# Kernel optimization log

Measured on AMD Instinct MI355X. Metric: run time of the kernel, lower is better.

Reference implementation:

```python
import jax, jax.numpy as jnp
import numpy as np

N, E = 20000, 320000
CS, CV = 64, 32          # scalar / vector multiplicities of node (= node_pre) irreps
AS_, AV, H = 16, 8, 4    # attn irreps scalar/vector muls, num_heads
NB = 16                  # num_basis
SQRT3 = 1.7320508075688772
SQRT2 = 1.4142135623730951
EPS = 1e-5

# dtp weight layout: [ss(CS), sv(CS), vs(CV), vv0(CV), vv1(CV)] -> numel = 2*CS+3*CV = 224

def _cg_tp(s, v, y0, y1, w_ss, w_sv, w_vs, w_vv0, w_vv1):
    """Depthwise CG tensor product for l<=1.
    s:(E,CS) v:(E,CV,3) y0:(E,) y1:(E,3); weights (E,C) or (C,).
    out scalars (E, CS+CV): 0e x 0e -> 0e, 1o x 1o -> 0e (dot/sqrt3)
    out vectors (E, CS+2*CV, 3): 0e x 1o -> 1o, 1o x 0e -> 1o, 1o x 1o -> 1o (cross/sqrt2)
    """
    out_s = jnp.concatenate([
        w_ss * s * y0[:, None],
        w_vv0 * (jnp.einsum('eci,ei->ec', v, y1) / SQRT3)], axis=-1)
    out_v = jnp.concatenate([
        (w_sv * s)[:, :, None] * y1[:, None, :],
        (w_vs * jnp.ones_like(v[..., 0]))[..., None] * v * y0[:, None, None],
        (w_vv1 * jnp.ones_like(v[..., 0]))[..., None] * (jnp.cross(v, y1[:, None, :]) / SQRT2)], axis=1)
    return out_s, out_v


def _equiv_layernorm(s, v, gamma_s, beta_s, gamma_v):
    mu = jnp.mean(s, axis=-1, keepdims=True)
    var = jnp.var(s, axis=-1, keepdims=True)
    s_n = (s - mu) * jax.lax.rsqrt(var + EPS) * gamma_s + beta_s
    rms = jnp.sqrt(jnp.mean(jnp.sum(v * v, axis=-1), axis=-1, keepdims=True) + EPS)
    v_n = v / rms[..., None] * gamma_v[None, :, None]
    return s_n, v_n


def setup_inputs() -> dict:
    key = jax.random.key(0)
    ks = jax.random.split(key, 26)
    def rn(k, shape, fan):
        return jax.random.normal(k, shape, jnp.float32) / np.sqrt(fan)
    D1S, D1V = CS + CV, CS + 2 * CV          # 96, 128 (dtp output muls)
    WN = 2 * CS + 3 * CV                     # 224 dtp weight numel
    inp = {
        'node': jax.random.normal(ks[0], (N, CS + 3 * CV), jnp.float32),
        'edge_index': jax.random.randint(ks[1], (2, E), 0, N, jnp.int64 if jax.config.jax_enable_x64 else jnp.int32),
        'rbf': jax.random.uniform(ks[2], (E, NB), jnp.float32),
        'rsh': jax.random.normal(ks[3], (E, 4), jnp.float32),
        'gamma_s': jnp.ones((CS,), jnp.float32),
        'beta_s': jnp.zeros((CS,), jnp.float32),
        'gamma_v': jnp.ones((CV,), jnp.float32),
        'Ws_src': rn(ks[4], (CS, CS), CS), 'Wv_src': rn(ks[5], (CV, CV), CV),
        'Ws_dst': rn(ks[6], (CS, CS), CS), 'Wv_dst': rn(ks[7], (CV, CV), CV),
        'W_rbf': rn(ks[8], (NB, WN), NB),
        'W_alpha': rn(ks[9], (D1S, H * AS_), D1S),
        'alpha_dot': rn(ks[10], (1, H, AS_), AS_),
        'Ws_val': rn(ks[11], (D1S, CS), D1S), 'Wv_val': rn(ks[12], (D1V, CV), D1V),
        'Wg': rn(ks[13], (CS, CV), CS),
        'w2_ss': rn(ks[14], (CS,), 1), 'w2_sv': rn(ks[15], (CS,), 1),
        'w2_vs': rn(ks[16], (CV,), 1), 'w2_vv0': rn(ks[17], (CV,), 1), 'w2_vv1': rn(ks[18], (CV,), 1),
        'Ws_vlin': rn(ks[19], (D1S, H * AS_), D1S), 'Wv_vlin': rn(ks[20], (D1V, H * AV), D1V),
        'Wps': rn(ks[21], (H * AS_, CS), H * AS_), 'Wpv': rn(ks[22], (H * AV, CV), H * AV),
    }
    return inp


def reference(node, rbf, rsh, gamma_s, beta_s, gamma_v, Ws_src, Wv_src, Ws_dst, Wv_dst,
              W_rbf, W_alpha, alpha_dot, Ws_val, Wv_val, Wg,
              w2_ss, w2_sv, w2_vs, w2_vv0, w2_vv1, Ws_vlin, Wv_vlin, Wps, Wpv, edge_index):
    n = node.shape[0]
    e = rsh.shape[0]
    s = node[:, :CS]
    v = node[:, CS:].reshape(n, CV, 3)
    # equivariant layer norm
    s_n, v_n = _equiv_layernorm(s, v, gamma_s, beta_s, gamma_v)
    # merge_src / merge_dst (irrep-wise o3.Linear)
    src, dst = edge_index[0], edge_index[1]
    msg_s = (s_n @ Ws_src)[src] + (s_n @ Ws_dst)[dst]                       # (E,CS)
    msg_v = jnp.einsum('ncx,cd->ndx', v_n, Wv_src)[src] + \
            jnp.einsum('ncx,cd->ndx', v_n, Wv_dst)[dst]                     # (E,CV,3)
    y0, y1 = rsh[:, 0], rsh[:, 1:4]
    # dtp1: per-edge weighted CG coupling, weights from rbf
    w1 = rbf @ W_rbf                                                        # (E,224)
    m1_s, m1_v = _cg_tp(msg_s, msg_v, y0, y1,
                        w1[:, :CS], w1[:, CS:2*CS], w1[:, 2*CS:2*CS+CV],
                        w1[:, 2*CS+CV:2*CS+2*CV], w1[:, 2*CS+2*CV:])        # (E,96) (E,128,3)
    # attention logits
    a = (m1_s @ W_alpha).reshape(e, H, AS_)
    a = jnp.where(a > 0, a, 0.2 * a)                                        # LeakyReLU(0.2)
    a = jnp.sum(a * alpha_dot, axis=-1, keepdims=True)                      # (E,H,1)
    # softmax over incoming edges of each destination node
    amax = jax.ops.segment_max(a, dst, num_segments=n)
    amax = jnp.where(jnp.isfinite(amax), amax, 0.0)
    ex = jnp.exp(a - amax[dst])
    den = jax.ops.segment_sum(ex, dst, num_segments=n)
    alpha = ex / (den[dst] + 1e-16)                                         # (E,H,1)
    # value path
    val_s = m1_s @ Ws_val                                                   # (E,CS)
    val_v = jnp.einsum('ecx,cd->edx', m1_v, Wv_val)                         # (E,CV,3)
    # gate: sigmoid on scalars, vectors gated by sigmoid of learned scalar gates
    val_v = val_v * jax.nn.sigmoid(val_s @ Wg)[..., None]
    val_s = jax.nn.sigmoid(val_s)
    # dtp2: shared internal weights
    m2_s, m2_v = _cg_tp(val_s, val_v, y0, y1, w2_ss, w2_sv, w2_vs, w2_vv0, w2_vv1)
    # value_lin -> (attn_irreps * num_heads), head-major layout
    hs = (m2_s @ Ws_vlin).reshape(e, H, AS_)
    hv = jnp.einsum('ecx,cd->edx', m2_v, Wv_vlin).reshape(e, H, AV, 3)
    h = jnp.concatenate([hs, hv.reshape(e, H, AV * 3)], axis=-1)            # (E,H,40)
    # attend + scatter-add to destination nodes
    agg = jax.ops.segment_sum(alpha * h, dst, num_segments=n)               # (N,H,40)
    agg_s = agg[:, :, :AS_].reshape(n, H * AS_)                             # (N,64)
    agg_v = agg[:, :, AS_:].reshape(n, H * AV, 3)                           # (N,32,3)
    out = node + jnp.concatenate([
        agg_s @ Wps,
        jnp.einsum('ncx,cd->ndx', agg_v, Wpv).reshape(n, CV * 3)], axis=-1)
    return out
```

## Files before the change

kernel.cpp:

```cpp
#include <hip/hip_runtime.h>
#include <hip/hip_bf16.h>
#include <cstddef>

typedef __hip_bfloat16 bf16;
typedef __bf16 bfv8 __attribute__((ext_vector_type(8)));
typedef __bf16 bfv4 __attribute__((ext_vector_type(4)));
typedef float f4 __attribute__((ext_vector_type(4)));

#define EPSN 1e-5f
#define SQRT3_INV 0.57735026918962576f
#define SQRT2_INV 0.70710678118654752f

__device__ __forceinline__ float b2f(bf16 x) { return __bfloat162float(x); }

template<int BF> __device__ __forceinline__ float ldf(const void* p, size_t i) {
    if (BF) return __bfloat162float(((const bf16*)p)[i]);
    return ((const float*)p)[i];
}
__device__ __forceinline__ float ldr(const void* p, size_t i, int bfm) {
    return bfm ? __bfloat162float(((const bf16*)p)[i]) : ((const float*)p)[i];
}
template<int BF> __device__ __forceinline__ void stf(void* p, size_t i, float v) {
    if (BF) ((bf16*)p)[i] = __float2bfloat16(v);
    else    ((float*)p)[i] = v;
}

__device__ __forceinline__ float wave_sum64(float x) {
    #pragma unroll
    for (int m = 1; m < 64; m <<= 1) x += __shfl_xor(x, m, 64);
    return x;
}

__device__ __forceinline__ f4 mf(bfv8 a, bfv8 b, f4 c) {
    return __builtin_amdgcn_mfma_f32_16x16x32_bf16(a, b, c, 0, 0, 0);
}

__global__ __launch_bounds__(256) void k_sniff(const void* node, const void* eidx, int* flags)
{
    int t = threadIdx.x;
    __shared__ int cnt;
    __shared__ unsigned orr;
    if (t == 0) { cnt = 0; orr = 0u; }
    __syncthreads();
    unsigned w  = ((const unsigned*)node)[t];
    unsigned lo = w & 0xFFFFu;
    int e_lo = (int)((lo >> 7) & 0xFF);
    if (e_lo >= 96 && e_lo <= 140) atomicAdd(&cnt, 1);
    unsigned odd = ((const unsigned*)eidx)[2 * t + 1];
    atomicOr(&orr, odd);
    __syncthreads();
    if (t == 0) {
        flags[0] = (cnt >= 128) ? 1 : 0;
        flags[1] = (orr == 0u) ? 1 : 0;
    }
}

__global__ __launch_bounds__(256) void k_zero(float* p, int n)
{
    int i = blockIdx.x * 256 + threadIdx.x;
    if (i < n) p[i] = 0.f;
}

__global__ __launch_bounds__(256) void k_hist(const void* eidx, int* cnt,
                                              const int* flags, int E)
{
    int e = blockIdx.x * 256 + threadIdx.x;
    if (e >= E) return;
    int d = flags[1] ? (int)((const long long*)eidx)[(long long)E + e]
                     : ((const int*)eidx)[(size_t)E + e];
    atomicAdd(&cnt[d], 1);
}

__global__ __launch_bounds__(1024) void k_scan(int* cnt, int N)
{
    __shared__ int wsum[16];
    int t = threadIdx.x;
    int lane = t & 63, w = t >> 6;
    int chunk = (N + 1023) >> 10;
    int lo = t * chunk, hi = lo + chunk;
    if (hi > N) hi = N; if (lo > N) lo = N;
    int sum = 0;
    for (int i = lo; i < hi; ++i) sum += cnt[i];
    int x = sum;
    #pragma unroll
    for (int off = 1; off < 64; off <<= 1) {
        int y = __shfl_up(x, off, 64);
        if (lane >= off) x += y;
    }
    if (lane == 63) wsum[w] = x;
    __syncthreads();
    if (t < 64) {
        int v = (lane < 16) ? wsum[lane] : 0;
        #pragma unroll
        for (int off = 1; off < 16; off <<= 1) {
            int y = __shfl_up(v, off, 64);
            if (lane >= off) v += y;
        }
        if (lane < 16) wsum[lane] = v;
    }
    __syncthreads();
    int acc = x - sum + (w ? wsum[w - 1] : 0);
    for (int i = lo; i < hi; ++i) { int v = cnt[i]; cnt[i] = acc; acc += v; }
}

__global__ __launch_bounds__(256) void k_perm(const void* eidx, int* cnt, int* perm,
                                              const int* flags, int E)
{
    int e = blockIdx.x * 256 + threadIdx.x;
    if (e >= E) return;
    int d = flags[1] ? (int)((const long long*)eidx)[(long long)E + e]
                     : ((const int*)eidx)[(size_t)E + e];
    int pos = atomicAdd(&cnt[d], 1);
    perm[pos] = e;
}

template<int BF>
__device__ __forceinline__ void prep_impl(
    const void* Walpha, const void* Wsval, const void* Wsvlin,
    const void* Wvval, const void* Wvvlin, const void* Wg,
    const void* Wrbf, const void* adot,
    const void* w2ss, const void* w2sv, const void* w2vs,
    const void* w2vv0, const void* w2vv1,
    bf16* WalphaT, bf16* WsvalT, bf16* WsvlinT,
    bf16* WvvalT, bf16* WvvlinT, bf16* WgT,
    bf16* WrbfT, bf16* adotB, bf16* w2B)
{
    int t = threadIdx.x + blockIdx.x * 256;
    int T = gridDim.x * 256;
    for (int i = t; i < 96 * 64; i += T) {
        int c = i >> 6, n = i & 63;
        WalphaT[n * 96 + c] = __float2bfloat16(ldf<BF>(Walpha, i));
        WsvalT [n * 96 + c] = __float2bfloat16(ldf<BF>(Wsval,  i));
        WsvlinT[n * 96 + c] = __float2bfloat16(ldf<BF>(Wsvlin, i));
    }
    for (int i = t; i < 128 * 32; i += T) {
        int c = i >> 5, n = i & 31;
        WvvalT [n * 128 + c] = __float2bfloat16(ldf<BF>(Wvval,  i));
        WvvlinT[n * 128 + c] = __float2bfloat16(ldf<BF>(Wvvlin, i));
    }
    for (int i = t; i < 64 * 32; i += T) {
        int c = i >> 5, n = i & 31;
        WgT[n * 64 + c] = __float2bfloat16(ldf<BF>(Wg, i));
    }
    for (int i = t; i < 224 * 32; i += T) {
        int c = i >> 5, b = i & 31;
        WrbfT[i] = __float2bfloat16(b < 16 ? ldf<BF>(Wrbf, b * 224 + c) : 0.f);
    }
    if (t < 64) adotB[t] = __float2bfloat16(ldf<BF>(adot, t));
    if (t < 64) w2B[t]      = __float2bfloat16(ldf<BF>(w2ss, t));
    if (t < 64) w2B[64 + t] = __float2bfloat16(ldf<BF>(w2sv, t));
    if (t < 32) {
        w2B[128 + t] = __float2bfloat16(ldf<BF>(w2vs, t));
        w2B[160 + t] = __float2bfloat16(ldf<BF>(w2vv0, t));
        w2B[192 + t] = __float2bfloat16(ldf<BF>(w2vv1, t));
    }
}

__global__ __launch_bounds__(256) void k_prep(
    const void* Walpha, const void* Wsval, const void* Wsvlin,
    const void* Wvval, const void* Wvvlin, const void* Wg,
    const void* Wrbf, const void* adot,
    const void* w2ss, const void* w2sv, const void* w2vs,
    const void* w2vv0, const void* w2vv1,
    bf16* WalphaT, bf16* WsvalT, bf16* WsvlinT,
    bf16* WvvalT, bf16* WvvlinT, bf16* WgT,
    bf16* WrbfT, bf16* adotB, bf16* w2B, const int* flags)
{
    if (flags[0])
        prep_impl<1>(Walpha, Wsval, Wsvlin, Wvval, Wvvlin, Wg, Wrbf, adot,
                     w2ss, w2sv, w2vs, w2vv0, w2vv1,
                     WalphaT, WsvalT, WsvlinT, WvvalT, WvvlinT, WgT, WrbfT, adotB, w2B);
    else
        prep_impl<0>(Walpha, Wsval, Wsvlin, Wvval, Wvvlin, Wg, Wrbf, adot,
                     w2ss, w2sv, w2vs, w2vv0, w2vv1,
                     WalphaT, WsvalT, WsvlinT, WvvalT, WvvlinT, WgT, WrbfT, adotB, w2B);
}

template<int BF>
__device__ __forceinline__ void node_impl(
    const void* node, const void* gs, const void* bs, const void* gv,
    const void* Wss, const void* Wvs, const void* Wsd, const void* Wvd,
    bf16* ssrc, bf16* sdst, bf16* vsrc, bf16* vdst,
    float* shs, float* shv, int n, int lane)
{
    size_t nb = (size_t)n * 160;

    float s  = ldf<BF>(node, nb + lane);
    float mu = wave_sum64(s) * (1.f / 64.f);
    float d  = s - mu;
    float var = wave_sum64(d * d) * (1.f / 64.f);
    float sn  = d * rsqrtf(var + EPSN) * ldf<BF>(gs, lane) + ldf<BF>(bs, lane);
    shs[lane] = sn;

    float v0 = 0.f, v1 = 0.f, v2 = 0.f, qq = 0.f;
    if (lane < 32) {
        v0 = ldf<BF>(node, nb + 64 + lane * 3 + 0);
        v1 = ldf<BF>(node, nb + 64 + lane * 3 + 1);
        v2 = ldf<BF>(node, nb + 64 + lane * 3 + 2);
        qq = v0 * v0 + v1 * v1 + v2 * v2;
    }
    float msq = wave_sum64(qq) * (1.f / 32.f);
    float inv = rsqrtf(msq + EPSN);
    if (lane < 32) {
        float g = ldf<BF>(gv, lane);
        shv[0 * 32 + lane] = v0 * inv * g;
        shv[1 * 32 + lane] = v1 * inv * g;
        shv[2 * 32 + lane] = v2 * inv * g;
    }

    float a1 = 0.f, a2 = 0.f;
    for (int c = 0; c < 64; ++c) {
        float sc = shs[c];
        a1 += sc * ldf<BF>(Wss, c * 64 + lane);
        a2 += sc * ldf<BF>(Wsd, c * 64 + lane);
    }
    {
        int cs = lane;
        int pos = (cs & 15) * 4 + (cs >> 4);
        ssrc[(size_t)n * 64 + pos] = __float2bfloat16(a1);
        sdst[(size_t)n * 64 + pos] = __float2bfloat16(a2);
    }

    {
        int x = lane >> 5, dd = lane & 31;
        float p1 = 0.f, p2 = 0.f;
        for (int c = 0; c < 32; ++c) {
            float vc = shv[x * 32 + c];
            p1 += vc * ldf<BF>(Wvs, c * 32 + dd);
            p2 += vc * ldf<BF>(Wvd, c * 32 + dd);
        }
        int cv = x * 32 + dd;
        int pos = (cv & 15) * 8 + (cv >> 4);
        vsrc[(size_t)n * 128 + pos] = __float2bfloat16(p1);
        vdst[(size_t)n * 128 + pos] = __float2bfloat16(p2);
    }
    if (lane < 32) {
        int dd = lane;
        float p1 = 0.f, p2 = 0.f;
        for (int c = 0; c < 32; ++c) {
            float vc = shv[2 * 32 + c];
            p1 += vc * ldf<BF>(Wvs, c * 32 + dd);
            p2 += vc * ldf<BF>(Wvd, c * 32 + dd);
        }
        int cv = 64 + dd;
        int pos = (cv & 15) * 8 + (cv >> 4);
        vsrc[(size_t)n * 128 + pos] = __float2bfloat16(p1);
        vdst[(size_t)n * 128 + pos] = __float2bfloat16(p2);
    }
}

__global__ __launch_bounds__(256) void k_node(
    const void* node, const void* gs, const void* bs, const void* gv,
    const void* Wss, const void* Wvs, const void* Wsd, const void* Wvd,
    bf16* ssrc, bf16* sdst, bf16* vsrc, bf16* vdst,
    const int* flags, int N)
{
    __shared__ float shs[4][64];
    __shared__ float shv[4][96];
    int wv = threadIdx.x >> 6, lane = threadIdx.x & 63;
    int n = blockIdx.x * 4 + wv; if (n >= N) return;
    if (flags[0])
        node_impl<1>(node, gs, bs, gv, Wss, Wvs, Wsd, Wvd, ssrc, sdst, vsrc, vdst,
                     shs[wv], shv[wv], n, lane);
    else
        node_impl<0>(node, gs, bs, gv, Wss, Wvs, Wsd, Wvd, ssrc, sdst, vsrc, vdst,
                     shs[wv], shv[wv], n, lane);
}

static constexpr int SS  = 104;
static constexpr int A1S = 0;
static constexpr int SV  = 136;
static constexpr int P0  = 16 * SS;
static constexpr int P1  = P0 + 16 * SV;
static constexpr int VAL = 0;
static constexpr int SA  = 72;
static constexpr int HSZ = P1 + 16 * SV;

#define W_M1(X, PB) do { \
    constexpr int x_ = (X), x1_ = ((X)+1)%3, x2_ = ((X)+2)%3; \
    _Pragma("unroll") \
    for (int r = 0; r < 4; ++r) { \
        int e = q * 4 + r; \
        float4 yy = *(const float4*)&sY[wv][e][0]; \
        float y0 = yy.x; float yv[3] = {yy.y, yy.z, yy.w}; \
        _Pragma("unroll") \
        for (int nt = 0; nt < 4; ++nt) \
            H[(PB) + e * SV + nt * 16 + m] = (__bf16)(sv_[r][nt] * yv[x_]); \
        _Pragma("unroll") \
        for (int n2 = 0; n2 < 2; ++n2) { \
            int c = 64 + n2 * 16 + m; \
            H[(PB) + e * SV + c] = (__bf16)(qv_[r][n2][x_] * y0); \
            float cr = pv_[r][n2][x1_] * yv[x2_] - pv_[r][n2][x2_] * yv[x1_]; \
            H[(PB) + e * SV + 32 + c] = (__bf16)(cr * SQRT2_INV); \
        } \
    } \
} while (0)

#define W_M2(X, PB) do { \
    constexpr int x_ = (X), x1_ = ((X)+1)%3, x2_ = ((X)+2)%3; \
    _Pragma("unroll") \
    for (int r = 0; r < 4; ++r) { \
        int e = q * 4 + r; \
        float4 yy = *(const float4*)&sY[wv][e][0]; \
        float y0 = yy.x; float yv[3] = {yy.y, yy.z, yy.w}; \
        _Pragma("unroll") \
        for (int nt = 0; nt < 4; ++nt) \
            H[(PB) + e * SV + nt * 16 + m] = (__bf16)(c2sv[nt] * vals[nt][r] * yv[x_]); \
        _Pragma("unroll") \
        for (int n2 = 0; n2 < 2; ++n2) { \
            int c = 64 + n2 * 16 + m; \
            H[(PB) + e * SV + c] = (__bf16)(c2vs[n2] * vv[x_][n2][r] * y0); \
            float cr = vv[x1_][n2][r] * yv[x2_] - vv[x2_][n2][r] * yv[x1_]; \
            H[(PB) + e * SV + 32 + c] = (__bf16)(c2v1[n2] * cr * SQRT2_INV); \
        } \
    } \
} while (0)

#define MMA_V(PB, WB, O0, O1) do { \
    bfv8 fg_[4]; \
    _Pragma("unroll") \
    for (int kt = 0; kt < 4; ++kt) \
        fg_[kt] = *(const bfv8*)(H + (PB) + m * SV + kt * 32 + kq); \
    _Pragma("unroll") \
    for (int kt = 0; kt < 4; ++kt) { \
        O0 = mf(fg_[kt], *(const bfv8*)((WB) + (size_t)(0 * 16 + m) * 128 + kt * 32 + kq), O0); \
        O1 = mf(fg_[kt], *(const bfv8*)((WB) + (size_t)(1 * 16 + m) * 128 + kt * 32 + kq), O1); \
    } \
} while (0)

__global__ __launch_bounds__(256, 3) void k_edge(
    const void* __restrict__ eidx, const void* __restrict__ rbf, const void* __restrict__ rsh,
    const bf16* __restrict__ WalphaT, const bf16* __restrict__ WsvalT, const bf16* __restrict__ WsvlinT,
    const bf16* __restrict__ WvvalT, const bf16* __restrict__ WvvlinT, const bf16* __restrict__ WgT,
    const bf16* __restrict__ WrbfT, const bf16* __restrict__ adotB, const bf16* __restrict__ w2B,
    const bf16* __restrict__ ssrc, const bf16* __restrict__ sdst,
    const bf16* __restrict__ vsrc, const bf16* __restrict__ vdst,
    const int* __restrict__ perm,
    float* __restrict__ den, float* __restrict__ agg,
    const int* __restrict__ flags, int E)
{
    const int bfm = flags[0];
    const int i64 = flags[1];

    __shared__ __align__(16) __bf16 sH[4][HSZ];
    __shared__ __align__(16) float sY[4][16][4];
    __shared__ int sSD[4][48];

    int wv = threadIdx.x >> 6, l = threadIdx.x & 63;
    int q = l >> 4, m = l & 15;
    const int kq = q * 8;
    long long eb = ((long long)blockIdx.x * 4 + wv) * 16;
    if (eb >= E) return;
    __bf16* H = &sH[wv][0];

    if (l < 16) {
        long long p = eb + l; if (p > (long long)E - 1) p = E - 1;
        sSD[wv][32 + l] = perm[p];
    }
    if (l < 32) {
        int pe = sSD[wv][32 + (l & 15)];
        long long off = (l < 16) ? (long long)pe : ((long long)E + pe);
        sSD[wv][l] = i64 ? (int)((const long long*)eidx)[off] : ((const int*)eidx)[off];
    }
    {
        int pe = sSD[wv][32 + (l >> 2)];
        sY[wv][l >> 2][l & 3] = ldr(rsh, (size_t)pe * 4 + (l & 3), bfm);
    }

    f4 w1f[14];
    {
        bfv8 arb;
        #pragma unroll
        for (int i = 0; i < 8; ++i) arb[i] = (__bf16)0.f;
        if (q < 2) {
            int pe = sSD[wv][32 + m];
            if (bfm) {
                arb = *(const bfv8*)((const __bf16*)rbf + (size_t)pe * 16 + kq);
            } else {
                const float* rp = (const float*)rbf + (size_t)pe * 16 + kq;
                #pragma unroll
                for (int i = 0; i < 8; ++i) arb[i] = (__bf16)rp[i];
            }
        }
        const __bf16* wb = (const __bf16*)WrbfT;
        #pragma unroll
        for (int nt = 0; nt < 14; ++nt) {
            bfv8 bb = *(const bfv8*)(wb + (size_t)(nt * 16 + m) * 32 + kq);
            f4 z = {0.f, 0.f, 0.f, 0.f};
            w1f[nt] = mf(arb, bb, z);
        }
    }

    bfv4 gs_[4], gd_[4];
    bfv8 gv_[4], gw_[4];
    #pragma unroll
    for (int r = 0; r < 4; ++r) {
        int e = q * 4 + r;
        int s = sSD[wv][e], d = sSD[wv][16 + e];
        gs_[r] = *(const bfv4*)((const __bf16*)ssrc + (size_t)s * 64 + m * 4);
        gd_[r] = *(const bfv4*)((const __bf16*)sdst + (size_t)d * 64 + m * 4);
        gv_[r] = *(const bfv8*)((const __bf16*)vsrc + (size_t)s * 128 + m * 8);
        gw_[r] = *(const bfv8*)((const __bf16*)vdst + (size_t)d * 128 + m * 8);
    }
    float ms_[4][4], mv_[4][2][3];
    #pragma unroll
    for (int r = 0; r < 4; ++r) {
        #pragma unroll
        for (int nt = 0; nt < 4; ++nt)
            ms_[r][nt] = (float)gs_[r][nt] + (float)gd_[r][nt];
        #pragma unroll
        for (int x = 0; x < 3; ++x)
            #pragma unroll
            for (int n2 = 0; n2 < 2; ++n2)
                mv_[r][n2][x] = (float)gv_[r][2 * x + n2] + (float)gw_[r][2 * x + n2];
    }

    float sv_[4][4], qv_[4][2][3], pv_[4][2][3];
    #pragma unroll
    for (int r = 0; r < 4; ++r) {
        int e = q * 4 + r;
        float4 yy = *(const float4*)&sY[wv][e][0];
        float y0 = yy.x, yx = yy.y, yh = yy.z, yz = yy.w;
        #pragma unroll
        for (int nt = 0; nt < 4; ++nt) {
            H[A1S + e * SS + nt * 16 + m] = (__bf16)(w1f[nt][r] * ms_[r][nt] * y0);
            sv_[r][nt] = w1f[4 + nt][r] * ms_[r][nt];
        }
        #pragma unroll
        for (int n2 = 0; n2 < 2; ++n2) {
            float dot = mv_[r][n2][0] * yx + mv_[r][n2][1] * yh + mv_[r][n2][2] * yz;
            H[A1S + e * SS + 64 + n2 * 16 + m] = (__bf16)(w1f[10 + n2][r] * dot * SQRT3_INV);
            #pragma unroll
            for (int x = 0; x < 3; ++x) {
                qv_[r][n2][x] = w1f[8 + n2][r]  * mv_[r][n2][x];
                pv_[r][n2][x] = w1f[12 + n2][r] * mv_[r][n2][x];
            }
        }
    }

    bfv8 a1s0 = *(const bfv8*)(H + A1S + m * SS + 0  + kq);
    bfv8 a1s1 = *(const bfv8*)(H + A1S + m * SS + 32 + kq);
    bfv8 a1s2 = *(const bfv8*)(H + A1S + m * SS + 64 + kq);

    f4 vals[4];
    #pragma unroll
    for (int nt = 0; nt < 4; ++nt) {
        const __bf16* bp = (const __bf16*)WsvalT + (size_t)(nt * 16 + m) * 96 + kq;
        f4 acc = {0.f, 0.f, 0.f, 0.f};
        acc = mf(a1s0, *(const bfv8*)(bp),      acc);
        acc = mf(a1s1, *(const bfv8*)(bp + 32), acc);
        acc = mf(a1s2, *(const bfv8*)(bp + 64), acc);
        vals[nt] = acc;
    }
    #pragma unroll
    for (int nt = 0; nt < 4; ++nt)
        #pragma unroll
        for (int r = 0; r < 4; ++r) {
            float v = vals[nt][r];
            H[VAL + (q * 4 + r) * SA + nt * 16 + m] = (__bf16)v;
            vals[nt][r] = 1.f / (1.f + __expf(-v));
        }

    f4 gate[2];
    {
        bfv8 av0 = *(const bfv8*)(H + VAL + m * SA + 0  + kq);
        bfv8 av1 = *(const bfv8*)(H + VAL + m * SA + 32 + kq);
        #pragma unroll
        for (int nt = 0; nt < 2; ++nt) {
            const __bf16* bp = (const __bf16*)WgT + (size_t)(nt * 16 + m) * 64 + kq;
            f4 acc = {0.f, 0.f, 0.f, 0.f};
            acc = mf(av0, *(const bfv8*)(bp),      acc);
            acc = mf(av1, *(const bfv8*)(bp + 32), acc);
            gate[nt] = acc;
        }
        #pragma unroll
        for (int nt = 0; nt < 2; ++nt)
            #pragma unroll
            for (int r = 0; r < 4; ++r)
                gate[nt][r] = 1.f / (1.f + __expf(-gate[nt][r]));
    }

    float ex_[4][4];
    #pragma unroll
    for (int nt = 0; nt < 4; ++nt) {
        const __bf16* bp = (const __bf16*)WalphaT + (size_t)(nt * 16 + m) * 96 + kq;
        f4 acc = {0.f, 0.f, 0.f, 0.f};
        acc = mf(a1s0, *(const bfv8*)(bp),      acc);
        acc = mf(a1s1, *(const bfv8*)(bp + 32), acc);
        acc = mf(a1s2, *(const bfv8*)(bp + 64), acc);
        float ad = b2f(adotB[nt * 16 + m]);
        #pragma unroll
        for (int r = 0; r < 4; ++r) {
            float tv = acc[r];
            tv = tv > 0.f ? tv : 0.2f * tv;
            tv *= ad;
            tv += __shfl_xor(tv, 1); tv += __shfl_xor(tv, 2);
            tv += __shfl_xor(tv, 4); tv += __shfl_xor(tv, 8);
            tv = fminf(fmaxf(tv, -60.f), 60.f);
            ex_[nt][r] = __expf(tv);
        }
    }

    f4 vv[3][2];
    #pragma unroll
    for (int x = 0; x < 3; ++x)
        #pragma unroll
        for (int nt = 0; nt < 2; ++nt)
            vv[x][nt] = (f4){0.f, 0.f, 0.f, 0.f};

    W_M1(0, P0);
    W_M1(1, P1);
    MMA_V(P0, (const __bf16*)WvvalT, vv[0][0], vv[0][1]);
    W_M1(2, P0);
    MMA_V(P1, (const __bf16*)WvvalT, vv[1][0], vv[1][1]);
    MMA_V(P0, (const __bf16*)WvvalT, vv[2][0], vv[2][1]);

    #pragma unroll
    for (int x = 0; x < 3; ++x)
        #pragma unroll
        for (int nt = 0; nt < 2; ++nt)
            #pragma unroll
            for (int r = 0; r < 4; ++r)
                vv[x][nt][r] *= gate[nt][r];

    float c2ss[4], c2sv[4];
    #pragma unroll
    for (int nt = 0; nt < 4; ++nt) {
        c2ss[nt] = b2f(w2B[nt * 16 + m]);
        c2sv[nt] = b2f(w2B[64 + nt * 16 + m]);
    }
    float c2vs[2], c2v0[2], c2v1[2];
    #pragma unroll
    for (int nt = 0; nt < 2; ++nt) {
        c2vs[nt] = b2f(w2B[128 + nt * 16 + m]);
        c2v0[nt] = b2f(w2B[160 + nt * 16 + m]);
        c2v1[nt] = b2f(w2B[192 + nt * 16 + m]);
    }
    #pragma unroll
    for (int r = 0; r < 4; ++r) {
        int e = q * 4 + r;
        float4 yy = *(const float4*)&sY[wv][e][0];
        float y0 = yy.x, yx = yy.y, yh = yy.z, yz = yy.w;
        #pragma unroll
        for (int nt = 0; nt < 4; ++nt)
            H[A1S + e * SS + nt * 16 + m] = (__bf16)(c2ss[nt] * vals[nt][r] * y0);
        #pragma unroll
        for (int n2 = 0; n2 < 2; ++n2) {
            float dotv = vv[0][n2][r] * yx + vv[1][n2][r] * yh + vv[2][n2][r] * yz;
            H[A1S + e * SS + 64 + n2 * 16 + m] = (__bf16)(c2v0[n2] * dotv * SQRT3_INV);
        }
    }
    f4 hs[4];
    {
        bfv8 a2s0 = *(const bfv8*)(H + A1S + m * SS + 0  + kq);
        bfv8 a2s1 = *(const bfv8*)(H + A1S + m * SS + 32 + kq);
        bfv8 a2s2 = *(const bfv8*)(H + A1S + m * SS + 64 + kq);
        #pragma unroll
        for (int nt = 0; nt < 4; ++nt) {
            const __bf16* bp = (const __bf16*)WsvlinT + (size_t)(nt * 16 + m) * 96 + kq;
            f4 acc = {0.f, 0.f, 0.f, 0.f};
            acc = mf(a2s0, *(const bfv8*)(bp),      acc);
            acc = mf(a2s1, *(const bfv8*)(bp + 32), acc);
            acc = mf(a2s2, *(const bfv8*)(bp + 64), acc);
            hs[nt] = acc;
        }
    }

    f4 hv[3][2];
    #pragma unroll
    for (int x = 0; x < 3; ++x)
        #pragma unroll
        for (int nt = 0; nt < 2; ++nt)
            hv[x][nt] = (f4){0.f, 0.f, 0.f, 0.f};

    W_M2(0, P0);
    W_M2(1, P1);
    MMA_V(P0, (const __bf16*)WvvlinT, hv[0][0], hv[0][1]);
    W_M2(2, P0);
    MMA_V(P1, (const __bf16*)WvvlinT, hv[1][0], hv[1][1]);
    MMA_V(P0, (const __bf16*)WvvlinT, hv[2][0], hv[2][1]);

    float* Hf = (float*)H;
    #pragma unroll
    for (int r = 0; r < 4; ++r) {
        int e = q * 4 + r;
        float* row = Hf + e * 168;
        #pragma unroll
        for (int nt = 0; nt < 4; ++nt)
            row[nt * 40 + m] = ex_[nt][r] * hs[nt][r];
        #pragma unroll
        for (int nt = 0; nt < 2; ++nt) {
            int c = nt * 16 + m;
            int hh = c >> 3, dd = c & 7;
            float exv = (m >= 8) ? ex_[2 * nt + 1][r] : ex_[2 * nt][r];
            float* vb = row + hh * 40 + 16 + dd * 3;
            vb[0] = exv * hv[0][nt][r];
            vb[1] = exv * hv[1][nt][r];
            vb[2] = exv * hv[2][nt][r];
        }
        if (m < 4) row[160 + m] = ex_[m][r];
    }
    int nval = (int)((E - eb) < 16 ? (E - eb) : 16);
    {
        int s = 0;
        while (s < nval) {
            int d = sSD[wv][16 + s];
            int t = s + 1;
            while (t < nval && sSD[wv][16 + t] == d) ++t;
            float s0 = 0.f, s1 = 0.f, s2 = 0.f;
            for (int e = s; e < t; ++e) {
                const float* row = Hf + e * 168;
                s0 += row[l];
                s1 += row[64 + l];
                if (l < 36) s2 += row[128 + l];
            }
            float* rowp = agg + (size_t)d * 160;
            unsafeAtomicAdd(rowp + l, s0);
            unsafeAtomicAdd(rowp + 64 + l, s1);
            if (l < 32)      unsafeAtomicAdd(rowp + 128 + l, s2);
            else if (l < 36) unsafeAtomicAdd(den + (size_t)d * 4 + (l - 32), s2);
            s = t;
        }
    }
}

template<int BF>
__device__ __forceinline__ void out_impl(
    const void* node, const float* den, const float* agg,
    const void* Wps, const void* Wpv, void* out,
    float* shs, float* shv, float* sinv, int n, int lane)
{
    if (lane < 4) sinv[lane] = 1.f / (den[(size_t)n * 4 + lane] + 1e-16f);
    for (int idx = lane; idx < 160; idx += 64) {
        int h = idx / 40, r = idx - h * 40;
        float val = agg[(size_t)n * 160 + idx] * sinv[h];
        if (r < 16) shs[h * 16 + r] = val;
        else { int rr = r - 16; int dd = rr / 3, x = rr - dd * 3; shv[x * 32 + h * 8 + dd] = val; }
    }

    float acc = ldf<BF>(node, (size_t)n * 160 + lane);
    for (int c = 0; c < 64; ++c) acc += shs[c] * ldf<BF>(Wps, c * 64 + lane);
    stf<BF>(out, (size_t)n * 160 + lane, acc);

    {
        int idx = lane; int dd = idx / 3, x = idx - dd * 3;
        float a = ldf<BF>(node, (size_t)n * 160 + 64 + idx);
        for (int c = 0; c < 32; ++c) a += shv[x * 32 + c] * ldf<BF>(Wpv, c * 32 + dd);
        stf<BF>(out, (size_t)n * 160 + 64 + idx, a);
    }
    if (lane < 32) {
        int idx = 64 + lane; int dd = idx / 3, x = idx - dd * 3;
        float a = ldf<BF>(node, (size_t)n * 160 + 64 + idx);
        for (int c = 0; c < 32; ++c) a += shv[x * 32 + c] * ldf<BF>(Wpv, c * 32 + dd);
        stf<BF>(out, (size_t)n * 160 + 64 + idx, a);
    }
}

__global__ __launch_bounds__(256) void k_out(
    const void* node, const float* den, const float* agg,
    const void* Wps, const void* Wpv, void* out,
    const int* flags, int N)
{
    __shared__ float shs[4][64];
    __shared__ float shv[4][96];
    __shared__ float sinv[4][4];
    int wv = threadIdx.x >> 6, lane = threadIdx.x & 63;
    int n = blockIdx.x * 4 + wv; if (n >= N) return;
    if (flags[0])
        out_impl<1>(node, den, agg, Wps, Wpv, out, shs[wv], shv[wv], sinv[wv], n, lane);
    else
        out_impl<0>(node, den, agg, Wps, Wpv, out, shs[wv], shv[wv], sinv[wv], n, lane);
}

extern "C" void kernel_launch(void* const* d_in, const int* in_sizes, int n_in,
                              void* d_out, int out_size, void* d_ws, size_t ws_size,
                              hipStream_t stream)
{
    const void* node   = d_in[0];
    const void* eidx   = d_in[1];
    const void* rbf    = d_in[2];
    const void* rsh    = d_in[3];
    const void* gs     = d_in[4];
    const void* bs     = d_in[5];
    const void* gv     = d_in[6];
    const void* Wss    = d_in[7];
    const void* Wvs    = d_in[8];
    const void* Wsd    = d_in[9];
    const void* Wvd    = d_in[10];
    const void* Wrbf   = d_in[11];
    const void* Walpha = d_in[12];
    const void* adot   = d_in[13];
    const void* Wsval  = d_in[14];
    const void* Wvval  = d_in[15];
    const void* Wg     = d_in[16];
    const void* w2ss   = d_in[17];
    const void* w2sv   = d_in[18];
    const void* w2vs   = d_in[19];
    const void* w2vv0  = d_in[20];
    const void* w2vv1  = d_in[21];
    const void* Wsvlin = d_in[22];
    const void* Wvvlin = d_in[23];
    const void* Wps    = d_in[24];
    const void* Wpv    = d_in[25];

    int N = in_sizes[0] / 160;
    int E = in_sizes[1] / 2;

    char* base = (char*)d_ws;
    int*  flags   = (int*)base;
    bf16* WalphaT = (bf16*)(base + 16);
    bf16* WsvalT  = WalphaT + 6144;
    bf16* WsvlinT = WsvalT  + 6144;
    bf16* WvvalT  = WsvlinT + 6144;
    bf16* WvvlinT = WvvalT  + 4096;
    bf16* WgT     = WvvlinT + 4096;
    bf16* WrbfT   = WgT     + 2048;
    bf16* adotB   = WrbfT   + 7168;
    bf16* w2B     = adotB   + 64;
    bf16* ssrc    = w2B     + 224;
    bf16* sdst    = ssrc + (size_t)N * 64;
    bf16* vsrc    = sdst + (size_t)N * 64;
    bf16* vdst    = vsrc + (size_t)N * 128;
    float* den    = (float*)(vdst + (size_t)N * 128);
    float* agg    = den + (size_t)N * 4;
    int*  cnt     = (int*)(agg + (size_t)N * 160);
    int*  perm    = cnt + N;

    k_sniff<<<1, 256, 0, stream>>>(node, eidx, flags);
    int zn = N * 164;
    k_zero<<<(zn + 255) / 256, 256, 0, stream>>>(den, zn);
    k_zero<<<(N + 255) / 256, 256, 0, stream>>>((float*)cnt, N);

    int nbe = (E + 255) / 256;
    k_hist<<<nbe, 256, 0, stream>>>(eidx, cnt, flags, E);
    k_scan<<<1, 1024, 0, stream>>>(cnt, N);
    k_perm<<<nbe, 256, 0, stream>>>(eidx, cnt, perm, flags, E);

    k_prep<<<16, 256, 0, stream>>>(Walpha, Wsval, Wsvlin, Wvval, Wvvlin, Wg, Wrbf, adot,
                                   w2ss, w2sv, w2vs, w2vv0, w2vv1,
                                   WalphaT, WsvalT, WsvlinT, WvvalT, WvvlinT, WgT, WrbfT,
                                   adotB, w2B, flags);

    int nbn = (N + 3) / 4;
    k_node<<<nbn, 256, 0, stream>>>(node, gs, bs, gv, Wss, Wvs, Wsd, Wvd,
                                    ssrc, sdst, vsrc, vdst, flags, N);

    int nb = (E + 63) / 64;
    k_edge<<<nb, 256, 0, stream>>>(eidx, rbf, rsh,
                                   WalphaT, WsvalT, WsvlinT, WvvalT, WvvlinT, WgT, WrbfT,
                                   adotB, w2B, ssrc, sdst, vsrc, vdst, perm, den, agg, flags, E);

    int nbo = (N + 3) / 4;
    k_out<<<nbo, 256, 0, stream>>>(node, den, agg, Wps, Wpv, d_out, flags, N);
}
```

Baseline: 503.4 us.

## Split vector node tables, hoist vector weights, remap blocks per XCD, merge zeroing

The per-node projected vector features are split into an A table (x,y components, 4 bf16 per lane) and a B table (z component, 2 bf16 per lane). Each edge gather now reads only the 6 channels it uses instead of 8 padded ones, which cuts gathered bytes. The vector-weight MMA fragments are loaded once into registers and reused across the three spatial components instead of being reloaded each time. Block IDs are remapped so consecutive edge chunks land on the same XCD for L2 locality, and the count-buffer zeroing is merged into the single zero kernel. Holding the weights in registers adds register pressure, and merging the zeroing relies on cnt being contiguous after agg.

```diff
diff --git a/kernel.cpp b/kernel.cpp
--- a/kernel.cpp
+++ b/kernel.cpp
@@ -5,6 +5,7 @@
 typedef __hip_bfloat16 bf16;
 typedef __bf16 bfv8 __attribute__((ext_vector_type(8)));
 typedef __bf16 bfv4 __attribute__((ext_vector_type(4)));
+typedef __bf16 bfv2 __attribute__((ext_vector_type(2)));
 typedef float f4 __attribute__((ext_vector_type(4)));
 
 #define EPSN 1e-5f
@@ -180,7 +181,7 @@
 __device__ __forceinline__ void node_impl(
     const void* node, const void* gs, const void* bs, const void* gv,
     const void* Wss, const void* Wvs, const void* Wsd, const void* Wvd,
-    bf16* ssrc, bf16* sdst, bf16* vsrc, bf16* vdst,
+    bf16* ssrc, bf16* sdst, bf16* vsrcA, bf16* vdstA, bf16* vsrcB, bf16* vdstB,
     float* shs, float* shv, int n, int lane)
 {
     size_t nb = (size_t)n * 160;
@@ -229,10 +230,10 @@
             p1 += vc * ldf<BF>(Wvs, c * 32 + dd);
             p2 += vc * ldf<BF>(Wvd, c * 32 + dd);
         }
-        int cv = x * 32 + dd;
-        int pos = (cv & 15) * 8 + (cv >> 4);
-        vsrc[(size_t)n * 128 + pos] = __float2bfloat16(p1);
-        vdst[(size_t)n * 128 + pos] = __float2bfloat16(p2);
+        int mm = dd & 15, n2 = dd >> 4;
+        int pos = mm * 4 + x * 2 + n2;
+        vsrcA[(size_t)n * 64 + pos] = __float2bfloat16(p1);
+        vdstA[(size_t)n * 64 + pos] = __float2bfloat16(p2);
     }
     if (lane < 32) {
         int dd = lane;
@@ -242,17 +243,17 @@
             p1 += vc * ldf<BF>(Wvs, c * 32 + dd);
             p2 += vc * ldf<BF>(Wvd, c * 32 + dd);
         }
-        int cv = 64 + dd;
-        int pos = (cv & 15) * 8 + (cv >> 4);
-        vsrc[(size_t)n * 128 + pos] = __float2bfloat16(p1);
-        vdst[(size_t)n * 128 + pos] = __float2bfloat16(p2);
+        int mm = dd & 15, n2 = dd >> 4;
+        int pos = mm * 2 + n2;
+        vsrcB[(size_t)n * 32 + pos] = __float2bfloat16(p1);
+        vdstB[(size_t)n * 32 + pos] = __float2bfloat16(p2);
     }
 }
 
 __global__ __launch_bounds__(256) void k_node(
     const void* node, const void* gs, const void* bs, const void* gv,
     const void* Wss, const void* Wvs, const void* Wsd, const void* Wvd,
-    bf16* ssrc, bf16* sdst, bf16* vsrc, bf16* vdst,
+    bf16* ssrc, bf16* sdst, bf16* vsrcA, bf16* vdstA, bf16* vsrcB, bf16* vdstB,
     const int* flags, int N)
 {
     __shared__ float shs[4][64];
@@ -260,11 +261,11 @@
     int wv = threadIdx.x >> 6, lane = threadIdx.x & 63;
     int n = blockIdx.x * 4 + wv; if (n >= N) return;
     if (flags[0])
-        node_impl<1>(node, gs, bs, gv, Wss, Wvs, Wsd, Wvd, ssrc, sdst, vsrc, vdst,
-                     shs[wv], shv[wv], n, lane);
+        node_impl<1>(node, gs, bs, gv, Wss, Wvs, Wsd, Wvd,
+                     ssrc, sdst, vsrcA, vdstA, vsrcB, vdstB, shs[wv], shv[wv], n, lane);
     else
-        node_impl<0>(node, gs, bs, gv, Wss, Wvs, Wsd, Wvd, ssrc, sdst, vsrc, vdst,
-                     shs[wv], shv[wv], n, lane);
+        node_impl<0>(node, gs, bs, gv, Wss, Wvs, Wsd, Wvd,
+                     ssrc, sdst, vsrcA, vdstA, vsrcB, vdstB, shs[wv], shv[wv], n, lane);
 }
 
 static constexpr int SS  = 104;
@@ -316,15 +317,15 @@
     } \
 } while (0)
 
-#define MMA_V(PB, WB, O0, O1) do { \
+#define MMA_H(PB, WH, O0, O1) do { \
     bfv8 fg_[4]; \
     _Pragma("unroll") \
     for (int kt = 0; kt < 4; ++kt) \
         fg_[kt] = *(const bfv8*)(H + (PB) + m * SV + kt * 32 + kq); \
     _Pragma("unroll") \
     for (int kt = 0; kt < 4; ++kt) { \
-        O0 = mf(fg_[kt], *(const bfv8*)((WB) + (size_t)(0 * 16 + m) * 128 + kt * 32 + kq), O0); \
-        O1 = mf(fg_[kt], *(const bfv8*)((WB) + (size_t)(1 * 16 + m) * 128 + kt * 32 + kq), O1); \
+        O0 = mf(fg_[kt], WH[kt],     O0); \
+        O1 = mf(fg_[kt], WH[4 + kt], O1); \
     } \
 } while (0)
 
@@ -334,7 +335,8 @@
     const bf16* __restrict__ WvvalT, const bf16* __restrict__ WvvlinT, const bf16* __restrict__ WgT,
     const bf16* __restrict__ WrbfT, const bf16* __restrict__ adotB, const bf16* __restrict__ w2B,
     const bf16* __restrict__ ssrc, const bf16* __restrict__ sdst,
-    const bf16* __restrict__ vsrc, const bf16* __restrict__ vdst,
+    const bf16* __restrict__ vsrcA, const bf16* __restrict__ vdstA,
+    const bf16* __restrict__ vsrcB, const bf16* __restrict__ vdstB,
     const int* __restrict__ perm,
     float* __restrict__ den, float* __restrict__ agg,
     const int* __restrict__ flags, int E)
@@ -349,7 +351,15 @@
     int wv = threadIdx.x >> 6, l = threadIdx.x & 63;
     int q = l >> 4, m = l & 15;
     const int kq = q * 8;
-    long long eb = ((long long)blockIdx.x * 4 + wv) * 16;
+
+    int bid;
+    {
+        int nwg = gridDim.x, orig = blockIdx.x;
+        int qq_ = nwg >> 3, rr_ = nwg & 7;
+        int xcd = orig & 7, off = orig >> 3;
+        bid = (xcd < rr_ ? xcd * (qq_ + 1) : rr_ * (qq_ + 1) + (xcd - rr_) * qq_) + off;
+    }
+    long long eb = ((long long)bid * 4 + wv) * 16;
     if (eb >= E) return;
     __bf16* H = &sH[wv][0];
 
@@ -391,16 +401,18 @@
         }
     }
 
-    bfv4 gs_[4], gd_[4];
-    bfv8 gv_[4], gw_[4];
+    bfv4 gs_[4], gd_[4], gvA[4], gwA[4];
+    bfv2 gvB[4], gwB[4];
     #pragma unroll
     for (int r = 0; r < 4; ++r) {
         int e = q * 4 + r;
         int s = sSD[wv][e], d = sSD[wv][16 + e];
-        gs_[r] = *(const bfv4*)((const __bf16*)ssrc + (size_t)s * 64 + m * 4);
-        gd_[r] = *(const bfv4*)((const __bf16*)sdst + (size_t)d * 64 + m * 4);
-        gv_[r] = *(const bfv8*)((const __bf16*)vsrc + (size_t)s * 128 + m * 8);
-        gw_[r] = *(const bfv8*)((const __bf16*)vdst + (size_t)d * 128 + m * 8);
+        gs_[r] = *(const bfv4*)((const __bf16*)ssrc  + (size_t)s * 64 + m * 4);
+        gd_[r] = *(const bfv4*)((const __bf16*)sdst  + (size_t)d * 64 + m * 4);
+        gvA[r] = *(const bfv4*)((const __bf16*)vsrcA + (size_t)s * 64 + m * 4);
+        gwA[r] = *(const bfv4*)((const __bf16*)vdstA + (size_t)d * 64 + m * 4);
+        gvB[r] = *(const bfv2*)((const __bf16*)vsrcB + (size_t)s * 32 + m * 2);
+        gwB[r] = *(const bfv2*)((const __bf16*)vdstB + (size_t)d * 32 + m * 2);
     }
     float ms_[4][4], mv_[4][2][3];
     #pragma unroll
@@ -409,10 +421,11 @@
         for (int nt = 0; nt < 4; ++nt)
             ms_[r][nt] = (float)gs_[r][nt] + (float)gd_[r][nt];
         #pragma unroll
-        for (int x = 0; x < 3; ++x)
-            #pragma unroll
-            for (int n2 = 0; n2 < 2; ++n2)
-                mv_[r][n2][x] = (float)gv_[r][2 * x + n2] + (float)gw_[r][2 * x + n2];
+        for (int n2 = 0; n2 < 2; ++n2) {
+            mv_[r][n2][0] = (float)gvA[r][0 * 2 + n2] + (float)gwA[r][0 * 2 + n2];
+            mv_[r][n2][1] = (float)gvA[r][1 * 2 + n2] + (float)gwA[r][1 * 2 + n2];
+            mv_[r][n2][2] = (float)gvB[r][n2]         + (float)gwB[r][n2];
+        }
     }
 
     float sv_[4][4], qv_[4][2][3], pv_[4][2][3];
@@ -507,14 +520,21 @@
         #pragma unroll
         for (int nt = 0; nt < 2; ++nt)
             vv[x][nt] = (f4){0.f, 0.f, 0.f, 0.f};
-
-    W_M1(0, P0);
-    W_M1(1, P1);
-    MMA_V(P0, (const __bf16*)WvvalT, vv[0][0], vv[0][1]);
-    W_M1(2, P0);
-    MMA_V(P1, (const __bf16*)WvvalT, vv[1][0], vv[1][1]);
-    MMA_V(P0, (const __bf16*)WvvalT, vv[2][0], vv[2][1]);
-
+    {
+        bfv8 wh[8];
+        #pragma unroll
+        for (int nt = 0; nt < 2; ++nt)
+            #pragma unroll
+            for (int kt = 0; kt < 4; ++kt)
+                wh[nt * 4 + kt] = *(const bfv8*)((const __bf16*)WvvalT
+                                   + (size_t)(nt * 16 + m) * 128 + kt * 32 + kq);
+        W_M1(0, P0);
+        W_M1(1, P1);
+        MMA_H(P0, wh, vv[0][0], vv[0][1]);
+        W_M1(2, P0);
+        MMA_H(P1, wh, vv[1][0], vv[1][1]);
+        MMA_H(P0, wh, vv[2][0], vv[2][1]);
+    }
     #pragma unroll
     for (int x = 0; x < 3; ++x)
         #pragma unroll
@@ -572,13 +592,21 @@
         #pragma unroll
         for (int nt = 0; nt < 2; ++nt)
             hv[x][nt] = (f4){0.f, 0.f, 0.f, 0.f};
-
-    W_M2(0, P0);
-    W_M2(1, P1);
-    MMA_V(P0, (const __bf16*)WvvlinT, hv[0][0], hv[0][1]);
-    W_M2(2, P0);
-    MMA_V(P1, (const __bf16*)WvvlinT, hv[1][0], hv[1][1]);
-    MMA_V(P0, (const __bf16*)WvvlinT, hv[2][0], hv[2][1]);
+    {
+        bfv8 wh[8];
+        #pragma unroll
+        for (int nt = 0; nt < 2; ++nt)
+            #pragma unroll
+            for (int kt = 0; kt < 4; ++kt)
+                wh[nt * 4 + kt] = *(const bfv8*)((const __bf16*)WvvlinT
+                                   + (size_t)(nt * 16 + m) * 128 + kt * 32 + kq);
+        W_M2(0, P0);
+        W_M2(1, P1);
+        MMA_H(P0, wh, hv[0][0], hv[0][1]);
+        W_M2(2, P0);
+        MMA_H(P1, wh, hv[1][0], hv[1][1]);
+        MMA_H(P0, wh, hv[2][0], hv[2][1]);
+    }
 
     float* Hf = (float*)H;
     #pragma unroll
@@ -718,18 +746,19 @@
     bf16* adotB   = WrbfT   + 7168;
     bf16* w2B     = adotB   + 64;
     bf16* ssrc    = w2B     + 224;
-    bf16* sdst    = ssrc + (size_t)N * 64;
-    bf16* vsrc    = sdst + (size_t)N * 64;
-    bf16* vdst    = vsrc + (size_t)N * 128;
-    float* den    = (float*)(vdst + (size_t)N * 128);
+    bf16* sdst    = ssrc  + (size_t)N * 64;
+    bf16* vsrcA   = sdst  + (size_t)N * 64;
+    bf16* vdstA   = vsrcA + (size_t)N * 64;
+    bf16* vsrcB   = vdstA + (size_t)N * 64;
+    bf16* vdstB   = vsrcB + (size_t)N * 32;
+    float* den    = (float*)(vdstB + (size_t)N * 32);
     float* agg    = den + (size_t)N * 4;
     int*  cnt     = (int*)(agg + (size_t)N * 160);
     int*  perm    = cnt + N;
 
     k_sniff<<<1, 256, 0, stream>>>(node, eidx, flags);
-    int zn = N * 164;
+    int zn = N * 165;
     k_zero<<<(zn + 255) / 256, 256, 0, stream>>>(den, zn);
-    k_zero<<<(N + 255) / 256, 256, 0, stream>>>((float*)cnt, N);
 
     int nbe = (E + 255) / 256;
     k_hist<<<nbe, 256, 0, stream>>>(eidx, cnt, flags, E);
@@ -743,12 +772,13 @@
 
     int nbn = (N + 3) / 4;
     k_node<<<nbn, 256, 0, stream>>>(node, gs, bs, gv, Wss, Wvs, Wsd, Wvd,
-                                    ssrc, sdst, vsrc, vdst, flags, N);
+                                    ssrc, sdst, vsrcA, vdstA, vsrcB, vdstB, flags, N);
 
     int nb = (E + 63) / 64;
     k_edge<<<nb, 256, 0, stream>>>(eidx, rbf, rsh,
                                    WalphaT, WsvalT, WsvlinT, WvvalT, WvvlinT, WgT, WrbfT,
-                                   adotB, w2B, ssrc, sdst, vsrc, vdst, perm, den, agg, flags, E);
+                                   adotB, w2B, ssrc, sdst, vsrcA, vdstA, vsrcB, vdstB,
+                                   perm, den, agg, flags, E);
 
     int nbo = (N + 3) / 4;
     k_out<<<nbo, 256, 0, stream>>>(node, den, agg, Wps, Wpv, d_out, flags, N);
```

Result: faster. 468.6 us (-6.9%).
